# Performance work log

Hardware: AMD Instinct MI355X
Metric: run time of the kernel (lower is better)

Reference implementation:

```python
import jax, jax.numpy as jnp
import numpy as np

IN_FEATURES = 4096
OUT_FEATURES = 11008
GROUP_SIZE = 128
NUM_GROUPS = IN_FEATURES // GROUP_SIZE  # 32


def setup_inputs() -> dict:
    key = jax.random.key(0)
    k1, k2, k3, k4, k5 = jax.random.split(key, 5)
    x = jax.random.normal(k1, (4, 2048, IN_FEATURES), dtype=jnp.float32)
    # packed 4-bit weights: each int holds (high << 4) | low, values in [0, 256)
    qweight = jax.random.randint(k2, (IN_FEATURES // 2, OUT_FEATURES), 0, 256, dtype=jnp.int32)
    scales = jax.random.uniform(k3, (NUM_GROUPS, OUT_FEATURES), dtype=jnp.float32) * 0.01 + 1e-4
    zeros = jax.random.normal(k4, (NUM_GROUPS, OUT_FEATURES), dtype=jnp.float32) * 0.01
    bias = jax.random.normal(k5, (OUT_FEATURES,), dtype=jnp.float32) * 0.01
    return {"x": x, "qweight": qweight, "scales": scales, "zeros": zeros, "bias": bias}


def _dequantize(qweight, scales, zeros, dtype):
    # unpack two 4-bit values per byte; even input rows = low nibble, odd = high nibble
    low = ((qweight & 15) - 8).astype(dtype)          # [in/2, out]
    high = (((qweight >> 4) & 15) - 8).astype(dtype)  # [in/2, out]
    w = jnp.stack([low, high], axis=1).reshape(IN_FEATURES, OUT_FEATURES)
    # per-group affine dequant: w = q * scale + zero
    w = w.reshape(NUM_GROUPS, GROUP_SIZE, OUT_FEATURES)
    w = w * scales[:, None, :] + zeros[:, None, :]
    return w.reshape(IN_FEATURES, OUT_FEATURES)


def reference(x, qweight, scales, zeros, bias):
    weight = _dequantize(qweight, scales, zeros, x.dtype)  # [in, out]
    # F.linear(x, weight.T, bias) == x @ weight + bias
    return jnp.einsum('bsi,io->bso', x, weight) + bias
```

## Files before the change

### kernel.cpp

```cpp
#include <hip/hip_runtime.h>
#include <hip/hip_bf16.h>

#define IN_F 4096
#define OUT_F 11008
#define GSIZE 128
#define M_TOTAL 8192

typedef float f32x4 __attribute__((ext_vector_type(4)));
typedef float f32x16 __attribute__((ext_vector_type(16)));
typedef unsigned short u16x8 __attribute__((ext_vector_type(8)));
typedef unsigned int u32x4 __attribute__((ext_vector_type(4)));
typedef __bf16 bf16x8 __attribute__((ext_vector_type(8)));

#define ASG __attribute__((address_space(1)))
#define ASL __attribute__((address_space(3)))

__device__ __forceinline__ unsigned short f2bf(float f) {
    union { float f; unsigned int u; } v;
    v.f = f;
    unsigned int u = v.u;
    unsigned int r = (u + 0x7fffu + ((u >> 16) & 1u)) >> 16;
    return (unsigned short)r;
}


__global__ void convert_x_frag_kernel(const float* __restrict__ x,
                                      unsigned short* __restrict__ xb) {
    const int mf = blockIdx.x;
    const int r  = threadIdx.x >> 3;
    const int kb = (threadIdx.x & 7) * 8;
    const int k0 = blockIdx.y * 512;
    const float* src = x + (size_t)(mf * 32 + r) * IN_F;
    unsigned short* dst = xb + (size_t)mf * (IN_F / 16) * 512;
#pragma unroll
    for (int kk = 0; kk < 512; kk += 64) {
        const int k = k0 + kk + kb;
        f32x4 a = *(const f32x4*)(src + k);
        f32x4 b = *(const f32x4*)(src + k + 4);
        u16x8 v;
#pragma unroll
        for (int e = 0; e < 4; ++e) {
            v[e]     = f2bf(a[e]);
            v[e + 4] = f2bf(b[e]);
        }
        const int kf = k >> 4, q2 = (k >> 3) & 1;
        *(u16x8*)(dst + (size_t)kf * 512 + (q2 * 32 + r) * 8) = v;
    }
}

__global__ void dequant_w_frag_kernel(const int* __restrict__ qw,
                                      const float* __restrict__ scales,
                                      const float* __restrict__ zeros,
                                      unsigned short* __restrict__ wt) {
    const int n  = blockIdx.x * 256 + threadIdx.x;
    const int k0 = blockIdx.y * 32;
    const int g  = k0 >> 7;
    const float s = scales[(size_t)g * OUT_F + n];
    const float z = zeros[(size_t)g * OUT_F + n];

    unsigned short outv[32];
#pragma unroll
    for (int i = 0; i < 16; ++i) {
        int q = qw[(size_t)(k0 / 2 + i) * OUT_F + n];
        float lo = (float)((q & 15) - 8) * s + z;
        float hi = (float)(((q >> 4) & 15) - 8) * s + z;
        outv[2 * i]     = f2bf(lo);
        outv[2 * i + 1] = f2bf(hi);
    }
    const int nf = n >> 5, r32 = n & 31;
    unsigned short* base = wt + (size_t)nf * (IN_F / 16) * 512 +
                           (size_t)(k0 >> 4) * 512;
    const u16x8* sv = (const u16x8*)outv;
#pragma unroll
    for (int c = 0; c < 4; ++c)
        *(u16x8*)(base + (c >> 1) * 512 + ((c & 1) * 32 + r32) * 8) = sv[c];
}

__global__ void dequant_w_rowmajor_kernel(const int* __restrict__ qw,
                                          const float* __restrict__ scales,
                                          const float* __restrict__ zeros,
                                          unsigned short* __restrict__ wt) {
    const int n  = blockIdx.x * 256 + threadIdx.x;
    const int k0 = blockIdx.y * 32;
    const int g  = k0 >> 7;
    const float s = scales[(size_t)g * OUT_F + n];
    const float z = zeros[(size_t)g * OUT_F + n];

    unsigned short outv[32];
#pragma unroll
    for (int i = 0; i < 16; ++i) {
        int q = qw[(size_t)(k0 / 2 + i) * OUT_F + n];
        float lo = (float)((q & 15) - 8) * s + z;
        float hi = (float)(((q >> 4) & 15) - 8) * s + z;
        outv[2 * i]     = f2bf(lo);
        outv[2 * i + 1] = f2bf(hi);
    }
    u16x8* dst = (u16x8*)(wt + (size_t)n * IN_F + k0);
    const u16x8* src = (const u16x8*)outv;
#pragma unroll
    for (int i = 0; i < 4; ++i) dst[i] = src[i];
}

__global__ __launch_bounds__(512, 1)
void gemm_kc(const unsigned short* __restrict__ xb,
             const unsigned short* __restrict__ wt,
             const float* __restrict__ bias,
             float* __restrict__ out) {
    constexpr int NT = IN_F / 64;
    constexpr int NKF = IN_F / 16;
    __shared__ __attribute__((aligned(128))) unsigned short lds[65536];

    const int bid = (int)blockIdx.x;
    const int xcd = bid & 7;
    const int l   = bid >> 3;
    const int m0 = (xcd * 4 + (l & 3)) * 256;
    const int n0 = (l >> 2) * 256;

    const int tid  = threadIdx.x;
    const int lane = tid & 63;
    const int wave = tid >> 6;
    const int wr = wave >> 2;
    const int wc = wave & 3;
    const int r32 = lane & 31;
    const int q2  = lane >> 5;

    const ASG char* xbc = (const ASG char*)xb;
    const ASG char* wtc = (const ASG char*)wt;
    ASL char* ldsc = (ASL char*)lds;

    const int mfb = m0 >> 5;
    const int nfb = n0 >> 5;
    unsigned int oA[4], oB[4];
    int dA[4], dB[4];
#pragma unroll
    for (int kc = 0; kc < 4; ++kc) {
        oA[kc] = (unsigned int)(((mfb + wave) * NKF + kc) * 1024 + lane * 16);
        oB[kc] = (unsigned int)(((nfb + wave) * NKF + kc) * 1024 + lane * 16);
        dA[kc] = (wave * 4 + kc) * 1024;
        dB[kc] = 32768 + (wave * 4 + kc) * 1024;
    }

#define STG_Z(KC, P)                                                           \
    do {                                                                       \
        __builtin_amdgcn_global_load_lds(                                      \
            (ASG const unsigned int*)(xbc + oA[(KC)]),                         \
            (ASL unsigned int*)(ldsc + dA[(KC)] + (P) * 65536), 16, 0, 0);     \
        __builtin_amdgcn_global_load_lds(                                      \
            (ASG const unsigned int*)(wtc + oB[(KC)]),                         \
            (ASL unsigned int*)(ldsc + dB[(KC)] + (P) * 65536), 16, 0, 0);     \
        oA[(KC)] += 4096;                                                      \
        oB[(KC)] += 4096;                                                      \
    } while (0)

#define BAR()                                                                  \
    do {                                                                       \
        __builtin_amdgcn_sched_barrier(0);                                     \
        __builtin_amdgcn_s_barrier();                                          \
        __builtin_amdgcn_sched_barrier(0);                                     \
    } while (0)

    bf16x8 afR[2][4];
    bf16x8 bfR[2][2];
    f32x16 acc[4][2];
#pragma unroll
    for (int i = 0; i < 4; ++i)
#pragma unroll
        for (int j = 0; j < 2; ++j) acc[i][j] = (f32x16)0.0f;

#define READ_KC(P, KC, S)                                                      \
    do {                                                                       \
        const unsigned short* _b = lds + (P) * 32768 + lane * 8;               \
        _Pragma("unroll") for (int _m = 0; _m < 4; ++_m)                       \
            afR[S][_m] = *(const bf16x8*)(_b +                                 \
                (((wr * 4 + _m) * 4 + (KC)) << 9));                            \
        _Pragma("unroll") for (int _n = 0; _n < 2; ++_n)                       \
            bfR[S][_n] = *(const bf16x8*)(_b + 16384 +                         \
                (((wc * 2 + _n) * 4 + (KC)) << 9));                            \
    } while (0)

#define QUAD_KC(S)                                                             \
    do {                                                                       \
        __builtin_amdgcn_s_setprio(1);                                         \
        _Pragma("unroll") for (int _m = 0; _m < 4; ++_m)                       \
        _Pragma("unroll") for (int _n = 0; _n < 2; ++_n)                       \
            acc[_m][_n] = __builtin_amdgcn_mfma_f32_32x32x16_bf16(             \
                afR[S][_m], bfR[S][_n], acc[_m][_n], 0, 0, 0);                 \
        __builtin_amdgcn_s_setprio(0);                                         \
    } while (0)

#pragma unroll
    for (int kc = 0; kc < 4; ++kc) STG_Z(kc, 0);
#pragma unroll
    for (int kc = 0; kc < 4; ++kc) STG_Z(kc, 1);
    __builtin_amdgcn_sched_barrier(0);
    asm volatile("s_waitcnt vmcnt(8)" ::: "memory");
    BAR();
    READ_KC(0, 0, 0);
    BAR();

#pragma unroll 1
    for (int tt = 0; tt < NT; tt += 2) {
        const bool g2 = (tt + 2 < NT);
        const bool g3 = (tt + 3 < NT);
        QUAD_KC(0); READ_KC(0, 1, 1); if (g2) STG_Z(0, 0); BAR();
        QUAD_KC(1); READ_KC(0, 2, 0); if (g2) STG_Z(1, 0); BAR();
        QUAD_KC(0); READ_KC(0, 3, 1); if (g2) STG_Z(2, 0); BAR();
        QUAD_KC(1);
        if (g2) STG_Z(3, 0);
        __builtin_amdgcn_sched_barrier(0);
        if (tt < NT - 2) {
            asm volatile("s_waitcnt vmcnt(8)" ::: "memory");
        } else {
            asm volatile("s_waitcnt vmcnt(0)" ::: "memory");
        }
        __builtin_amdgcn_sched_barrier(0);
        READ_KC(1, 0, 0);
        BAR();
        QUAD_KC(0); READ_KC(1, 1, 1); if (g3) STG_Z(0, 1); BAR();
        QUAD_KC(1); READ_KC(1, 2, 0); if (g3) STG_Z(1, 1); BAR();
        QUAD_KC(0); READ_KC(1, 3, 1); if (g3) STG_Z(2, 1); BAR();
        QUAD_KC(1);
        if (g3) STG_Z(3, 1);
        __builtin_amdgcn_sched_barrier(0);
        if (tt + 1 < NT - 2) {
            asm volatile("s_waitcnt vmcnt(8)" ::: "memory");
        } else {
            asm volatile("s_waitcnt vmcnt(0)" ::: "memory");
        }
        __builtin_amdgcn_sched_barrier(0);
        if (g2) READ_KC(0, 0, 0);
        BAR();
    }

#pragma unroll
    for (int nf = 0; nf < 2; ++nf) {
        const int col = n0 + wc * 64 + nf * 32 + r32;
        const float bv = bias[col];
#pragma unroll
        for (int mf = 0; mf < 4; ++mf) {
            const int row0 = m0 + wr * 128 + mf * 32 + q2 * 4;
#pragma unroll
            for (int r = 0; r < 16; ++r) {
                const int row = row0 + (r & 3) + ((r >> 2) << 3);
                __builtin_nontemporal_store(acc[mf][nf][r] + bv,
                                            &out[(size_t)row * OUT_F + col]);
            }
        }
    }
#undef STG_Z
#undef BAR
#undef READ_KC
#undef QUAD_KC
}

template <bool PREW>
__global__ __launch_bounds__(256, 2)
void gemm_kernel(const float* __restrict__ x,
                 const unsigned short* __restrict__ wt,
                 const int* __restrict__ qw,
                 const float* __restrict__ scales,
                 const float* __restrict__ zeros,
                 const float* __restrict__ bias,
                 float* __restrict__ out) {
    constexpr int BM = 128, BN = 128, BK = 64;
    constexpr int LDK = BK + 8;
    constexpr int NT = IN_F / BK;

    __shared__ unsigned short As[BM * LDK];
    __shared__ unsigned short Bs[BN * LDK];

    const int bid = blockIdx.x;
    constexpr int NB_N = OUT_F / BN;
    const int m0 = (bid / NB_N) * BM;
    const int n0 = (bid % NB_N) * BN;

    const int tid  = threadIdx.x;
    const int lane = tid & 63;
    const int wave = tid >> 6;
    const int wr = wave >> 1, wc = wave & 1;

    const int st_row = tid >> 3;
    const int st_col = (tid & 7) * 8;

    f32x4 areg[4][2];
    u32x4 breg[4];
    int   qreg[16];
    float s_, z_;
    const int b_n  = tid & 127;
    const int b_kp = (tid >> 7) * 16;

    auto load_tile = [&](int kt) {
        {
            const float* base = x + (size_t)m0 * IN_F + (size_t)kt * BK + st_col;
#pragma unroll
            for (int p = 0; p < 4; ++p) {
                const float* rp = base + (size_t)(p * 32 + st_row) * IN_F;
                areg[p][0] = *(const f32x4*)rp;
                areg[p][1] = *(const f32x4*)(rp + 4);
            }
        }
        if constexpr (PREW) {
            const unsigned short* base = wt + (size_t)n0 * IN_F + (size_t)kt * BK + st_col;
#pragma unroll
            for (int p = 0; p < 4; ++p)
                breg[p] = *(const u32x4*)(base + (size_t)(p * 32 + st_row) * IN_F);
        } else {
            const int kp0 = kt * (BK / 2) + b_kp;
#pragma unroll
            for (int i = 0; i < 16; ++i)
                qreg[i] = qw[(size_t)(kp0 + i) * OUT_F + n0 + b_n];
            const int g = (kt * BK) >> 7;
            s_ = scales[(size_t)g * OUT_F + n0 + b_n];
            z_ = zeros[(size_t)g * OUT_F + n0 + b_n];
        }
    };

    auto write_lds = [&]() {
#pragma unroll
        for (int p = 0; p < 4; ++p) {
            u16x8 v;
#pragma unroll
            for (int e = 0; e < 4; ++e) {
                v[e]     = f2bf(areg[p][0][e]);
                v[e + 4] = f2bf(areg[p][1][e]);
            }
            *(u16x8*)(&As[(p * 32 + st_row) * LDK + st_col]) = v;
        }
        if constexpr (PREW) {
#pragma unroll
            for (int p = 0; p < 4; ++p)
                *(u32x4*)(&Bs[(p * 32 + st_row) * LDK + st_col]) = breg[p];
        } else {
            unsigned short tmp[32];
#pragma unroll
            for (int i = 0; i < 16; ++i) {
                int q = qreg[i];
                tmp[2 * i]     = f2bf((float)((q & 15) - 8) * s_ + z_);
                tmp[2 * i + 1] = f2bf((float)(((q >> 4) & 15) - 8) * s_ + z_);
            }
            const u16x8* srcv = (const u16x8*)tmp;
#pragma unroll
            for (int i = 0; i < 4; ++i)
                *(u16x8*)(&Bs[b_n * LDK + 2 * b_kp + 8 * i]) = srcv[i];
        }
    };

    f32x4 acc[4][4];
#pragma unroll
    for (int i = 0; i < 4; ++i)
#pragma unroll
        for (int j = 0; j < 4; ++j) acc[i][j] = (f32x4)0.0f;

    load_tile(0);

#pragma unroll 1
    for (int kt = 0; kt < NT; ++kt) {
        __syncthreads();
        write_lds();
        __syncthreads();
        if (kt + 1 < NT) load_tile(kt + 1);

#pragma unroll
        for (int kk = 0; kk < 2; ++kk) {
            const int kidx = kk * 32 + ((lane >> 4) << 3);
            bf16x8 afv[4], bfv[4];
#pragma unroll
            for (int i = 0; i < 4; ++i)
                afv[i] = *(const bf16x8*)(&As[(wr * 64 + i * 16 + (lane & 15)) * LDK + kidx]);
#pragma unroll
            for (int j = 0; j < 4; ++j)
                bfv[j] = *(const bf16x8*)(&Bs[(wc * 64 + j * 16 + (lane & 15)) * LDK + kidx]);
#pragma unroll
            for (int i = 0; i < 4; ++i)
#pragma unroll
                for (int j = 0; j < 4; ++j)
                    acc[i][j] = __builtin_amdgcn_mfma_f32_16x16x32_bf16(afv[i], bfv[j], acc[i][j], 0, 0, 0);
        }
    }

    const int orow_base = m0 + wr * 64 + ((lane >> 4) << 2);
    const int ocol_base = n0 + wc * 64 + (lane & 15);
#pragma unroll
    for (int j = 0; j < 4; ++j) {
        const float bv = bias[ocol_base + j * 16];
#pragma unroll
        for (int i = 0; i < 4; ++i) {
#pragma unroll
            for (int q = 0; q < 4; ++q) {
                out[(size_t)(orow_base + i * 16 + q) * OUT_F + (ocol_base + j * 16)] =
                    acc[i][j][q] + bv;
            }
        }
    }
}

extern "C" void kernel_launch(void* const* d_in, const int* in_sizes, int n_in,
                              void* d_out, int out_size, void* d_ws, size_t ws_size,
                              hipStream_t stream) {
    const float* x      = (const float*)d_in[0];
    const int*   qw     = (const int*)d_in[1];
    const float* scales = (const float*)d_in[2];
    const float* zeros  = (const float*)d_in[3];
    const float* bias   = (const float*)d_in[4];
    float* out = (float*)d_out;

    const size_t wt_bytes = (size_t)OUT_F * IN_F * sizeof(unsigned short);
    const size_t xb_bytes = (size_t)M_TOTAL * IN_F * sizeof(unsigned short);

    if (ws_size >= wt_bytes + xb_bytes) {
        unsigned short* wt = (unsigned short*)d_ws;
        unsigned short* xb = (unsigned short*)((char*)d_ws + wt_bytes);
        convert_x_frag_kernel<<<dim3(M_TOTAL / 32, 8), 256, 0, stream>>>(x, xb);
        dequant_w_frag_kernel<<<dim3(OUT_F / 256, IN_F / 32), 256, 0, stream>>>(qw, scales, zeros, wt);
        gemm_kc<<<(M_TOTAL / 256) * (OUT_F / 256), 512, 0, stream>>>(xb, wt, bias, out);
    } else if (ws_size >= wt_bytes) {
        unsigned short* wt = (unsigned short*)d_ws;
        dequant_w_rowmajor_kernel<<<dim3(OUT_F / 256, IN_F / 32), 256, 0, stream>>>(qw, scales, zeros, wt);
        gemm_kernel<true><<<(M_TOTAL / 128) * (OUT_F / 128), 256, 0, stream>>>(x, wt, qw, scales, zeros, bias, out);
    } else {
        gemm_kernel<false><<<(M_TOTAL / 128) * (OUT_F / 128), 256, 0, stream>>>(x, nullptr, qw, scales, zeros, bias, out);
    }
}
```

Before: 689.8 us.

## Load B fragments directly into registers instead of staging through LDS

```diff
diff --git a/kernel.cpp b/kernel.cpp
--- a/kernel.cpp
+++ b/kernel.cpp
@@ -102,13 +102,13 @@
 }
 
 __global__ __launch_bounds__(512, 1)
-void gemm_kc(const unsigned short* __restrict__ xb,
-             const unsigned short* __restrict__ wt,
-             const float* __restrict__ bias,
-             float* __restrict__ out) {
+void gemm_breg(const unsigned short* __restrict__ xb,
+               const unsigned short* __restrict__ wt,
+               const float* __restrict__ bias,
+               float* __restrict__ out) {
     constexpr int NT = IN_F / 64;
     constexpr int NKF = IN_F / 16;
-    __shared__ __attribute__((aligned(128))) unsigned short lds[65536];
+    __shared__ __attribute__((aligned(128))) unsigned short lds[32768];
 
     const int bid = (int)blockIdx.x;
     const int xcd = bid & 7;
@@ -125,31 +125,35 @@
     const int q2  = lane >> 5;
 
     const ASG char* xbc = (const ASG char*)xb;
-    const ASG char* wtc = (const ASG char*)wt;
     ASL char* ldsc = (ASL char*)lds;
 
     const int mfb = m0 >> 5;
     const int nfb = n0 >> 5;
-    unsigned int oA[4], oB[4];
-    int dA[4], dB[4];
+    unsigned int oA[4];
+    int dA[4];
 #pragma unroll
     for (int kc = 0; kc < 4; ++kc) {
         oA[kc] = (unsigned int)(((mfb + wave) * NKF + kc) * 1024 + lane * 16);
-        oB[kc] = (unsigned int)(((nfb + wave) * NKF + kc) * 1024 + lane * 16);
         dA[kc] = (wave * 4 + kc) * 1024;
-        dB[kc] = 32768 + (wave * 4 + kc) * 1024;
-    }
-
-#define STG_Z(KC, P)                                                           \
+    }
+
+    const char* pB = (const char*)wt + (size_t)(nfb + wc * 2) * NKF * 1024 +
+                     lane * 16;
+    unsigned int obOff = 0;
+
+#define STG_A(KC, P)                                                           \
     do {                                                                       \
         __builtin_amdgcn_global_load_lds(                                      \
             (ASG const unsigned int*)(xbc + oA[(KC)]),                         \
-            (ASL unsigned int*)(ldsc + dA[(KC)] + (P) * 65536), 16, 0, 0);     \
-        __builtin_amdgcn_global_load_lds(                                      \
-            (ASG const unsigned int*)(wtc + oB[(KC)]),                         \
-            (ASL unsigned int*)(ldsc + dB[(KC)] + (P) * 65536), 16, 0, 0);     \
+            (ASL unsigned int*)(ldsc + dA[(KC)] + (P) * 32768), 16, 0, 0);     \
         oA[(KC)] += 4096;                                                      \
-        oB[(KC)] += 4096;                                                      \
+    } while (0)
+
+#define BLOAD(DP, KC)                                                          \
+    do {                                                                       \
+        bfr[DP][0][KC] = *(const bf16x8*)(pB + obOff);                         \
+        bfr[DP][1][KC] = *(const bf16x8*)(pB + (NKF * 1024) + obOff);          \
+        obOff += 1024;                                                         \
     } while (0)
 
 #define BAR()                                                                  \
@@ -160,75 +164,72 @@
     } while (0)
 
     bf16x8 afR[2][4];
-    bf16x8 bfR[2][2];
+    bf16x8 bfr[2][2][4];
     f32x16 acc[4][2];
 #pragma unroll
     for (int i = 0; i < 4; ++i)
 #pragma unroll
         for (int j = 0; j < 2; ++j) acc[i][j] = (f32x16)0.0f;
 
-#define READ_KC(P, KC, S)                                                      \
+#define READ_AKC(P, KC, S)                                                     \
     do {                                                                       \
-        const unsigned short* _b = lds + (P) * 32768 + lane * 8;               \
+        const unsigned short* _b = lds + (P) * 16384 + lane * 8;               \
         _Pragma("unroll") for (int _m = 0; _m < 4; ++_m)                       \
             afR[S][_m] = *(const bf16x8*)(_b +                                 \
                 (((wr * 4 + _m) * 4 + (KC)) << 9));                            \
-        _Pragma("unroll") for (int _n = 0; _n < 2; ++_n)                       \
-            bfR[S][_n] = *(const bf16x8*)(_b + 16384 +                         \
-                (((wc * 2 + _n) * 4 + (KC)) << 9));                            \
     } while (0)
 
-#define QUAD_KC(S)                                                             \
+#define QUAD_KC(P, KC)                                                         \
     do {                                                                       \
         __builtin_amdgcn_s_setprio(1);                                         \
         _Pragma("unroll") for (int _m = 0; _m < 4; ++_m)                       \
         _Pragma("unroll") for (int _n = 0; _n < 2; ++_n)                       \
             acc[_m][_n] = __builtin_amdgcn_mfma_f32_32x32x16_bf16(             \
-                afR[S][_m], bfR[S][_n], acc[_m][_n], 0, 0, 0);                 \
+                afR[(KC) & 1][_m], bfr[P][_n][KC], acc[_m][_n], 0, 0, 0);      \
         __builtin_amdgcn_s_setprio(0);                                         \
     } while (0)
 
 #pragma unroll
-    for (int kc = 0; kc < 4; ++kc) STG_Z(kc, 0);
-#pragma unroll
-    for (int kc = 0; kc < 4; ++kc) STG_Z(kc, 1);
+    for (int kc = 0; kc < 4; ++kc) STG_A(kc, 0);
+#pragma unroll
+    for (int kc = 0; kc < 4; ++kc) STG_A(kc, 1);
+#pragma unroll
+    for (int kc = 0; kc < 4; ++kc) BLOAD(0, kc);
     __builtin_amdgcn_sched_barrier(0);
-    asm volatile("s_waitcnt vmcnt(8)" ::: "memory");
+    asm volatile("s_waitcnt vmcnt(12)" ::: "memory");
     BAR();
-    READ_KC(0, 0, 0);
+    READ_AKC(0, 0, 0);
     BAR();
 
 #pragma unroll 1
     for (int tt = 0; tt < NT; tt += 2) {
         const bool g2 = (tt + 2 < NT);
         const bool g3 = (tt + 3 < NT);
-        QUAD_KC(0); READ_KC(0, 1, 1); if (g2) STG_Z(0, 0); BAR();
-        QUAD_KC(1); READ_KC(0, 2, 0); if (g2) STG_Z(1, 0); BAR();
-        QUAD_KC(0); READ_KC(0, 3, 1); if (g2) STG_Z(2, 0); BAR();
-        QUAD_KC(1);
-        if (g2) STG_Z(3, 0);
+        QUAD_KC(0, 0); READ_AKC(0, 1, 1); BLOAD(1, 0); if (g2) STG_A(0, 0); BAR();
+        QUAD_KC(0, 1); READ_AKC(0, 2, 0); BLOAD(1, 1); if (g2) STG_A(1, 0); BAR();
+        QUAD_KC(0, 2); READ_AKC(0, 3, 1); BLOAD(1, 2); if (g2) STG_A(2, 0); BAR();
+        QUAD_KC(0, 3); BLOAD(1, 3); if (g2) STG_A(3, 0);
         __builtin_amdgcn_sched_barrier(0);
-        if (tt < NT - 2) {
-            asm volatile("s_waitcnt vmcnt(8)" ::: "memory");
+        if (g2) {
+            asm volatile("s_waitcnt vmcnt(12)" ::: "memory");
         } else {
             asm volatile("s_waitcnt vmcnt(0)" ::: "memory");
         }
+        BAR();
+        READ_AKC(1, 0, 0);
+        BAR();
+        QUAD_KC(1, 0); READ_AKC(1, 1, 1); if (g2) BLOAD(0, 0); if (g3) STG_A(0, 1); BAR();
+        QUAD_KC(1, 1); READ_AKC(1, 2, 0); if (g2) BLOAD(0, 1); if (g3) STG_A(1, 1); BAR();
+        QUAD_KC(1, 2); READ_AKC(1, 3, 1); if (g2) BLOAD(0, 2); if (g3) STG_A(2, 1); BAR();
+        QUAD_KC(1, 3); if (g2) BLOAD(0, 3); if (g3) STG_A(3, 1);
         __builtin_amdgcn_sched_barrier(0);
-        READ_KC(1, 0, 0);
-        BAR();
-        QUAD_KC(0); READ_KC(1, 1, 1); if (g3) STG_Z(0, 1); BAR();
-        QUAD_KC(1); READ_KC(1, 2, 0); if (g3) STG_Z(1, 1); BAR();
-        QUAD_KC(0); READ_KC(1, 3, 1); if (g3) STG_Z(2, 1); BAR();
-        QUAD_KC(1);
-        if (g3) STG_Z(3, 1);
-        __builtin_amdgcn_sched_barrier(0);
-        if (tt + 1 < NT - 2) {
-            asm volatile("s_waitcnt vmcnt(8)" ::: "memory");
+        if (g3) {
+            asm volatile("s_waitcnt vmcnt(12)" ::: "memory");
         } else {
             asm volatile("s_waitcnt vmcnt(0)" ::: "memory");
         }
-        __builtin_amdgcn_sched_barrier(0);
-        if (g2) READ_KC(0, 0, 0);
+        BAR();
+        if (g2) READ_AKC(0, 0, 0);
         BAR();
     }
 
@@ -247,9 +248,10 @@
             }
         }
     }
-#undef STG_Z
+#undef STG_A
+#undef BLOAD
 #undef BAR
-#undef READ_KC
+#undef READ_AKC
 #undef QUAD_KC
 }
 
@@ -412,7 +414,7 @@
         unsigned short* xb = (unsigned short*)((char*)d_ws + wt_bytes);
         convert_x_frag_kernel<<<dim3(M_TOTAL / 32, 8), 256, 0, stream>>>(x, xb);
         dequant_w_frag_kernel<<<dim3(OUT_F / 256, IN_F / 32), 256, 0, stream>>>(qw, scales, zeros, wt);
-        gemm_kc<<<(M_TOTAL / 256) * (OUT_F / 256), 512, 0, stream>>>(xb, wt, bias, out);
+        gemm_breg<<<(M_TOTAL / 256) * (OUT_F / 256), 512, 0, stream>>>(xb, wt, bias, out);
     } else if (ws_size >= wt_bytes) {
         unsigned short* wt = (unsigned short*)d_ws;
         dequant_w_rowmajor_kernel<<<dim3(OUT_F / 256, IN_F / 32), 256, 0, stream>>>(qw, scales, zeros, wt);
```

Result: slower. 761.0 us (+10.3%).

## Restructure GEMM main loop to one barrier per K-tile with single-tile prefetch

Applied to the files above, without the earlier changes.

```diff
diff --git a/kernel.cpp b/kernel.cpp
--- a/kernel.cpp
+++ b/kernel.cpp
@@ -102,10 +102,10 @@
 }
 
 __global__ __launch_bounds__(512, 1)
-void gemm_kc(const unsigned short* __restrict__ xb,
-             const unsigned short* __restrict__ wt,
-             const float* __restrict__ bias,
-             float* __restrict__ out) {
+void gemm_1bar(const unsigned short* __restrict__ xb,
+               const unsigned short* __restrict__ wt,
+               const float* __restrict__ bias,
+               float* __restrict__ out) {
     constexpr int NT = IN_F / 64;
     constexpr int NKF = IN_F / 16;
     __shared__ __attribute__((aligned(128))) unsigned short lds[65536];
@@ -152,9 +152,10 @@
         oB[(KC)] += 4096;                                                      \
     } while (0)
 
-#define BAR()                                                                  \
+#define TILE_SYNC()                                                            \
     do {                                                                       \
         __builtin_amdgcn_sched_barrier(0);                                     \
+        asm volatile("s_waitcnt vmcnt(0)" ::: "memory");                       \
         __builtin_amdgcn_s_barrier();                                          \
         __builtin_amdgcn_sched_barrier(0);                                     \
     } while (0)
@@ -188,48 +189,33 @@
         __builtin_amdgcn_s_setprio(0);                                         \
     } while (0)
 
+#define TILE_BODY(P, DO_STAGE)                                                 \
+    do {                                                                       \
+        if (DO_STAGE) {                                                        \
+            STG_Z(0, (P) ^ 1);                                                 \
+            STG_Z(1, (P) ^ 1);                                                 \
+            STG_Z(2, (P) ^ 1);                                                 \
+            STG_Z(3, (P) ^ 1);                                                 \
+        }                                                                      \
+        READ_KC(P, 0, 0);                                                      \
+        QUAD_KC(0);                                                            \
+        READ_KC(P, 1, 1);                                                      \
+        QUAD_KC(1);                                                            \
+        READ_KC(P, 2, 0);                                                      \
+        QUAD_KC(0);                                                            \
+        READ_KC(P, 3, 1);                                                      \
+        QUAD_KC(1);                                                            \
+        TILE_SYNC();                                                           \
+    } while (0)
+
 #pragma unroll
     for (int kc = 0; kc < 4; ++kc) STG_Z(kc, 0);
-#pragma unroll
-    for (int kc = 0; kc < 4; ++kc) STG_Z(kc, 1);
-    __builtin_amdgcn_sched_barrier(0);
-    asm volatile("s_waitcnt vmcnt(8)" ::: "memory");
-    BAR();
-    READ_KC(0, 0, 0);
-    BAR();
+    TILE_SYNC();
 
 #pragma unroll 1
     for (int tt = 0; tt < NT; tt += 2) {
-        const bool g2 = (tt + 2 < NT);
-        const bool g3 = (tt + 3 < NT);
-        QUAD_KC(0); READ_KC(0, 1, 1); if (g2) STG_Z(0, 0); BAR();
-        QUAD_KC(1); READ_KC(0, 2, 0); if (g2) STG_Z(1, 0); BAR();
-        QUAD_KC(0); READ_KC(0, 3, 1); if (g2) STG_Z(2, 0); BAR();
-        QUAD_KC(1);
-        if (g2) STG_Z(3, 0);
-        __builtin_amdgcn_sched_barrier(0);
-        if (tt < NT - 2) {
-            asm volatile("s_waitcnt vmcnt(8)" ::: "memory");
-        } else {
-            asm volatile("s_waitcnt vmcnt(0)" ::: "memory");
-        }
-        __builtin_amdgcn_sched_barrier(0);
-        READ_KC(1, 0, 0);
-        BAR();
-        QUAD_KC(0); READ_KC(1, 1, 1); if (g3) STG_Z(0, 1); BAR();
-        QUAD_KC(1); READ_KC(1, 2, 0); if (g3) STG_Z(1, 1); BAR();
-        QUAD_KC(0); READ_KC(1, 3, 1); if (g3) STG_Z(2, 1); BAR();
-        QUAD_KC(1);
-        if (g3) STG_Z(3, 1);
-        __builtin_amdgcn_sched_barrier(0);
-        if (tt + 1 < NT - 2) {
-            asm volatile("s_waitcnt vmcnt(8)" ::: "memory");
-        } else {
-            asm volatile("s_waitcnt vmcnt(0)" ::: "memory");
-        }
-        __builtin_amdgcn_sched_barrier(0);
-        if (g2) READ_KC(0, 0, 0);
-        BAR();
+        TILE_BODY(0, true);
+        TILE_BODY(1, (tt + 2 < NT));
     }
 
 #pragma unroll
@@ -248,9 +234,10 @@
         }
     }
 #undef STG_Z
-#undef BAR
+#undef TILE_SYNC
 #undef READ_KC
 #undef QUAD_KC
+#undef TILE_BODY
 }
 
 template <bool PREW>
@@ -412,7 +399,7 @@
         unsigned short* xb = (unsigned short*)((char*)d_ws + wt_bytes);
         convert_x_frag_kernel<<<dim3(M_TOTAL / 32, 8), 256, 0, stream>>>(x, xb);
         dequant_w_frag_kernel<<<dim3(OUT_F / 256, IN_F / 32), 256, 0, stream>>>(qw, scales, zeros, wt);
-        gemm_kc<<<(M_TOTAL / 256) * (OUT_F / 256), 512, 0, stream>>>(xb, wt, bias, out);
+        gemm_1bar<<<(M_TOTAL / 256) * (OUT_F / 256), 512, 0, stream>>>(xb, wt, bias, out);
     } else if (ws_size >= wt_bytes) {
         unsigned short* wt = (unsigned short*)d_ws;
         dequant_w_rowmajor_kernel<<<dim3(OUT_F / 256, IN_F / 32), 256, 0, stream>>>(qw, scales, zeros, wt);
```

Measured after the change: 710.9 us. +3.0%, slower.
